# Kernel tuning notes

Hardware: AMD Instinct MI355X
Metric: run time of the kernel (lower is better)

## Reference

```python
import jax, jax.numpy as jnp
import numpy as np

B, T, F, N = 262144, 3, 17, 8
EMBD = 32
DT = 0.2  # 25/5*0.04
EPS = 1e-8  # torch.cosine_similarity eps


def _mono(x, wi, bi, wo, bo):
    # monotonic_fun with increasing=False: relu(-Linear(x)) -> Linear
    h = jax.nn.relu(-(x @ wi.T + bi))  # (..., EMBD)
    return h @ wo.T + bo               # (..., 1)


def _cos(a, b):
    dot = jnp.sum(a * b, axis=-1)
    na = jnp.maximum(jnp.linalg.norm(a, axis=-1), EPS)
    nb = jnp.maximum(jnp.linalg.norm(b, axis=-1), EPS)
    return dot / (na * nb)


def _angle_clamp(vec, e, ang):
    # vec: (B,K,2), e: (B,2) -> keep forces within effective angle cone, sum over K
    keep = jnp.abs(_cos(e[:, None, :], vec)) > ang
    return jnp.sum(vec * keep[..., None], axis=1)


def setup_inputs() -> dict:
    key = jax.random.key(0)
    ks = jax.random.split(key, 8)
    ego = jax.random.normal(ks[0], (B, T, F), jnp.float32)
    ego = ego.at[:, :, 2:4].multiply(10.0)  # position scale
    nei = jax.random.normal(ks[1], (B, N, F), jnp.float32)
    nei = nei.at[:, :, 2:4].multiply(10.0).at[:, :, 4:6].multiply(0.1)
    border = jax.random.normal(ks[2], (4,), jnp.float32)
    attr_dest_para = jax.random.uniform(ks[3], (2,), jnp.float32) + 0.1  # relu(rand), keep away from 0 divisor
    eff_angle = jax.nn.sigmoid(jax.random.uniform(ks[4], (1,), jnp.float32))

    def mlp(k):
        k1, k2, k3, k4 = jax.random.split(k, 4)
        wi = jax.random.uniform(k1, (EMBD, 1), jnp.float32)      # clamped >= 0
        bi = jax.random.normal(k2, (EMBD,), jnp.float32) * 0.1
        wo = jax.random.uniform(k3, (1, EMBD), jnp.float32) * 0.1  # clamped >= 0
        bo = jax.random.normal(k4, (1,), jnp.float32) * 0.1
        return wi, bi, wo, bo

    an = mlp(ks[5])
    rn = mlp(ks[6])
    rb = mlp(ks[7])
    dl = mlp(jax.random.fold_in(key, 99))
    return dict(
        ego=ego, nei=nei, border=border,
        attr_dest_para=attr_dest_para, eff_angle=eff_angle,
        an_wi=an[0], an_bi=an[1], an_wo=an[2], an_bo=an[3],
        rn_wi=rn[0], rn_bi=rn[1], rn_wo=rn[2], rn_bo=rn[3],
        rb_wi=rb[0], rb_bi=rb[1], rb_wo=rb[2], rb_bo=rb[3],
        dl_wi=dl[0], dl_bi=dl[1], dl_wo=dl[2], dl_bo=dl[3],
    )


def reference(ego, nei, border, attr_dest_para, eff_angle,
              an_wi, an_bi, an_wo, an_bo,
              rn_wi, rn_bi, rn_wo, rn_bo,
              rb_wi, rb_bi, rb_wo, rb_bo,
              dl_wi, dl_bi, dl_wo, dl_bo):
    ego_last = ego[:, -1]  # (B,F)

    # --- attr_destination (desired_velocity=None branch) ---
    v34 = ego_last[:, 3:5]
    dv = jnp.stack([jnp.linalg.norm(v34, axis=-1),
                    jnp.zeros(ego.shape[0], ego.dtype)], axis=1)  # (B,2)
    f_dest = ((attr_dest_para[1] * dv - v34) / attr_dest_para[0])[:, None, :]  # (B,1,2)

    # --- attr_repu_neighbors ---
    r = nei[:, :, 2:4] - ego_last[:, None, 2:4]  # (B,N,2)
    mask = nei[:, :, 2:4] == 0                    # (B,N,2)
    r_norm = jnp.linalg.norm(r, axis=-1, keepdims=True)  # (B,N,1)

    # neighbor durality: quirky use of batch element 1, shared across batch
    ids_last = ego[1, -1, 8:-1]  # (8,) neighbor-id columns
    dur = jnp.zeros(N, ego.dtype)
    for t in range(ego.shape[1]):
        dur = dur + jnp.isin(ids_last, ego[1, t, 8:-1]).astype(ego.dtype)

    f_attr = _mono(r_norm, an_wi, an_bi, an_wo, an_bo) * r / r_norm \
             * _mono(dur[:, None], dl_wi, dl_bi, dl_wo, dl_bo)  # (B,N,2)*(N,1)
    f_attr = jnp.where(mask, 0.0, f_attr)

    v_nei = nei[:, :, 4:6]
    b = r_norm \
        + jnp.sum((r + v_nei * DT) ** 2, axis=-1, keepdims=True) \
        - jnp.sum((v_nei * DT) ** 2, axis=-1, keepdims=True)
    b = jnp.sqrt(b) / 2
    f_repu = _mono(b, rn_wi, rn_bi, rn_wo, rn_bo) * r / r_norm
    f_repu = jnp.where(mask, 0.0, f_repu)

    # --- repu_borders (select_lane = [0, -1]) ---
    rb_all = ego_last[:, 3, None] - border        # (B,4)
    rbv = jnp.stack([rb_all[:, 0], rb_all[:, -1]], axis=1)  # (B,2)
    rbn = jnp.abs(rbv)
    f_bor = _mono(rbn[..., None], rb_wi, rb_bi, rb_wo, rb_bo) * (rbv / rbn)[..., None]  # (B,2,1)
    f_bor = jnp.concatenate([jnp.zeros_like(f_bor), f_bor], axis=-1)  # (B,2,2): [0, fy]

    # --- angle clamp + integrate ---
    e = ego_last[:, 4:6]
    e = e / jnp.linalg.norm(e, axis=1, keepdims=True)
    a = (_angle_clamp(f_dest, e, eff_angle)
         + _angle_clamp(f_attr, e, eff_angle) + _angle_clamp(f_repu, e, eff_angle)
         + _angle_clamp(f_bor, e, eff_angle))
    v = ego_last[:, 2:4] + a * DT
    s = ego_last[:, :2] + v * DT
    return jnp.concatenate([s, v, a], axis=1)  # (B,6)
```

## Files before the change

kernel.cpp:

```cpp
#include <hip/hip_runtime.h>

#define DTC 0.2f
#define EPSC 1e-8f


__device__ __forceinline__ float mono_eval(const float* __restrict__ kn, float x) {
    int i = (kn[15] <= x) ? 16 : 0;
    i += (kn[i + 7] <= x) ? 8 : 0;
    i += (kn[i + 3] <= x) ? 4 : 0;
    i += (kn[i + 1] <= x) ? 2 : 0;
    i += (kn[i] <= x) ? 1 : 0;
    return -fmaf(kn[32 + i], x, kn[65 + i]);
}

__global__ __launch_bounds__(256, 6) void sfm_fused(
    const float* __restrict__ ego, const float* __restrict__ nei,
    const float* __restrict__ border, const float* __restrict__ adp,
    const float* __restrict__ eang,
    const float* __restrict__ an_wi, const float* __restrict__ an_bi,
    const float* __restrict__ an_wo, const float* __restrict__ an_bo,
    const float* __restrict__ rn_wi, const float* __restrict__ rn_bi,
    const float* __restrict__ rn_wo, const float* __restrict__ rn_bo,
    const float* __restrict__ rb_wi, const float* __restrict__ rb_bi,
    const float* __restrict__ rb_wo, const float* __restrict__ rb_bo,
    const float* __restrict__ dl_wi, const float* __restrict__ dl_bi,
    const float* __restrict__ dl_wo, const float* __restrict__ dl_bo,
    float* __restrict__ out, int Bn)
{
    __shared__ __align__(16) float sw[360];
    __shared__ __align__(16) float snei[4352];
    __shared__ __align__(16) float sego[1632];
    __shared__ __align__(16) float sout[192];

    int t = threadIdx.x;

    if (t < 96) {
        int f = t >> 5, k = t & 31;
        const float* wip = (f == 0) ? an_wi : ((f == 1) ? rn_wi : rb_wi);
        const float* bip = (f == 0) ? an_bi : ((f == 1) ? rn_bi : rb_bi);
        const float* wop = (f == 0) ? an_wo : ((f == 1) ? rn_wo : rb_wo);
        float wi = wip[k], bi = bip[k], wo = wop[k];
        snei[t]       = -bi / wi;
        snei[96 + t]  = wi * wo;
        snei[192 + t] = wo * bi;
    }
    __syncthreads();
    if (t < 96) {
        int f = t >> 5, k = t & 31;
        float my = snei[t];
        int rank = 0;
        for (int m = 0; m < 32; ++m) {
            float o = snei[f * 32 + m];
            rank += (o < my || (o == my && m < k)) ? 1 : 0;
        }
        snei[288 + f * 32 + rank] = my;
        snei[384 + f * 32 + rank] = snei[96 + t];
        snei[480 + f * 32 + rank] = snei[192 + t];
    }
    __syncthreads();
    if (t < 96) {
        int f = t >> 5, p = t & 31;
        float sw_ = 0.f, sb_ = 0.f;
        for (int m = p; m < 32; ++m) { sw_ += snei[384 + f * 32 + m]; sb_ += snei[480 + f * 32 + m]; }
        int base = 16 + f * 112;
        sw[base + p]      = snei[288 + f * 32 + p];
        sw[base + 32 + p] = sw_;
        sw[base + 65 + p] = sb_;
        if (p == 0) { sw[base + 64] = 0.f; sw[base + 97] = 0.f; }
    }
    if (t >= 96 && t < 104) {
        int j = t - 96;
        const float* base = ego + 51;
        float idv = base[2 * 17 + 8 + j];
        float dur = 0.f;
        for (int tt = 0; tt < 3; ++tt) {
            bool fo = false;
            for (int m = 0; m < 8; ++m) fo = fo || (idv == base[tt * 17 + 8 + m]);
            dur += fo ? 1.f : 0.f;
        }
        float acc = 0.f;
        for (int k = 0; k < 32; ++k)
            acc = fmaf(dl_wo[k], fmaxf(0.f, -fmaf(dl_wi[k], dur, dl_bi[k])), acc);
        sw[j] = acc + dl_bo[0];
    }
    if (t == 104) sw[352] = an_bo[0];
    if (t == 105) sw[353] = rn_bo[0];
    if (t == 106) sw[354] = rb_bo[0];
    if (t == 107) sw[355] = adp[0];
    if (t == 108) sw[356] = adp[1];
    if (t == 109) sw[357] = eang[0];
    if (t == 110) sw[358] = border[0];
    if (t == 111) sw[359] = border[3];
    __syncthreads();

    int l   = t & 7;
    int r32 = t >> 3;
    long long nTiles = ((long long)Bn + 31) >> 5;

    for (long long tt = blockIdx.x; tt < nTiles; tt += gridDim.x) {
        {
            const float4* nsrc = (const float4*)nei + tt * 1088;
            float4* nd = (float4*)snei;
#pragma unroll
            for (int i = 0; i < 5; ++i) {
                int idx = t + 256 * i;
                if (idx < 1088 && tt * 1088 + idx < (long long)Bn * 34) nd[idx] = nsrc[idx];
            }
            const float4* esrc = (const float4*)ego + tt * 408;
            float4* ed = (float4*)sego;
#pragma unroll
            for (int i = 0; i < 2; ++i) {
                int idx = t + 256 * i;
                if (idx < 408 && tt * 408 + idx < ((long long)Bn * 51) / 4) ed[idx] = esrc[idx];
            }
        }
        __syncthreads();

        long long row = tt * 32 + r32;
        if (row < Bn) {
            const float* eg = sego + 51 * r32 + 34;
            float g0 = eg[0], g1 = eg[1], g2 = eg[2], g3 = eg[3], g4 = eg[4], g5 = eg[5];

            const float* nr = snei + 136 * r32 + 17 * l + 2;
            float nx = nr[0], ny = nr[1], vx = nr[2], vy = nr[3];

            float Rx = nx - g2, Ry = ny - g3;
            float rr = sqrtf(Rx * Rx + Ry * Ry);
            float ax = fmaf(vx, DTC, Rx), ay = fmaf(vy, DTC, Ry);
            float wx = vx * DTC, wy = vy * DTC;
            float bb = sqrtf(rr + ax * ax + ay * ay - wx * wx - wy * wy) * 0.5f;

            float an_bo_v = sw[352], rn_bo_v = sw[353], rb_bo_v = sw[354];
            float p0 = sw[355], p1 = sw[356], ang = sw[357];
            float rb0 = g3 - sw[358], rb1 = g3 - sw[359];
            float rbn0 = fabsf(rb0), rbn1 = fabsf(rb1);

            float fA = mono_eval(sw + 16, rr) + an_bo_v;
            float fR = mono_eval(sw + 128, bb) + rn_bo_v;
            float xb = (l == 1) ? rbn1 : rbn0;
            float vB = 0.f;
            if (l < 2) vB = mono_eval(sw + 240, xb) + rb_bo_v;
            int lb = (t & 63) & ~7;
            float vB0 = __shfl(vB, lb + 0, 64);
            float vB1 = __shfl(vB, lb + 1, 64);

            float elen = sqrtf(g4 * g4 + g5 * g5);
            float ex = g4 / elen, ey = g5 / elen;
            float na = fmaxf(sqrtf(ex * ex + ey * ey), EPSC);

            float axs = 0.f, ays = 0.f;
#define CLAMP_ADD(VX, VY)                                                   \
            {                                                               \
                float _vx = (VX), _vy = (VY);                               \
                float _nv = fmaxf(sqrtf(_vx * _vx + _vy * _vy), EPSC);      \
                float _c = (ex * _vx + ey * _vy) / (na * _nv);              \
                if (fabsf(_c) > ang) { axs += _vx; ays += _vy; }            \
            }

            float mfx = (nx == 0.f) ? 0.f : 1.f;
            float mfy = (ny == 0.f) ? 0.f : 1.f;

            { float coef = fA / rr * sw[l];  CLAMP_ADD(coef * Rx * mfx, coef * Ry * mfy); }
            { float coef = fR / rr;          CLAMP_ADD(coef * Rx * mfx, coef * Ry * mfy); }

#pragma unroll
            for (int m = 1; m < 8; m <<= 1) {
                axs += __shfl_xor(axs, m, 64);
                ays += __shfl_xor(ays, m, 64);
            }

            if (l == 0) {
                float dvn = sqrtf(g3 * g3 + g4 * g4);
                CLAMP_ADD((p1 * dvn - g3) / p0, -g4 / p0);
                CLAMP_ADD(0.f, vB0 * (rb0 / rbn0));
                CLAMP_ADD(0.f, vB1 * (rb1 / rbn1));

                float vxo = fmaf(axs, DTC, g2);
                float vyo = fmaf(ays, DTC, g3);
                float* op = sout + 6 * r32;
                op[0] = fmaf(vxo, DTC, g0);
                op[1] = fmaf(vyo, DTC, g1);
                op[2] = vxo; op[3] = vyo;
                op[4] = axs; op[5] = ays;
            }
#undef CLAMP_ADD
        }
        __syncthreads();

        if (t < 48) {
            long long o4 = tt * 48 + t;
            if (o4 < ((long long)Bn * 6) / 4) ((float4*)out)[o4] = ((const float4*)sout)[t];
        }
        __syncthreads();
    }
}

extern "C" void kernel_launch(void* const* d_in, const int* in_sizes, int n_in,
                              void* d_out, int out_size, void* d_ws, size_t ws_size,
                              hipStream_t stream) {
    const float* ego    = (const float*)d_in[0];
    const float* nei    = (const float*)d_in[1];
    const float* border = (const float*)d_in[2];
    const float* adp    = (const float*)d_in[3];
    const float* eang   = (const float*)d_in[4];
    const float* an_wi  = (const float*)d_in[5];
    const float* an_bi  = (const float*)d_in[6];
    const float* an_wo  = (const float*)d_in[7];
    const float* an_bo  = (const float*)d_in[8];
    const float* rn_wi  = (const float*)d_in[9];
    const float* rn_bi  = (const float*)d_in[10];
    const float* rn_wo  = (const float*)d_in[11];
    const float* rn_bo  = (const float*)d_in[12];
    const float* rb_wi  = (const float*)d_in[13];
    const float* rb_bi  = (const float*)d_in[14];
    const float* rb_wo  = (const float*)d_in[15];
    const float* rb_bo  = (const float*)d_in[16];
    const float* dl_wi  = (const float*)d_in[17];
    const float* dl_bi  = (const float*)d_in[18];
    const float* dl_wo  = (const float*)d_in[19];
    const float* dl_bo  = (const float*)d_in[20];
    float* out = (float*)d_out;
    (void)d_ws; (void)ws_size;

    int Bn = in_sizes[0] / (3 * 17);

    sfm_fused<<<1536, 256, 0, stream>>>(ego, nei, border, adp, eang,
                                        an_wi, an_bi, an_wo, an_bo,
                                        rn_wi, rn_bi, rn_wo, rn_bo,
                                        rb_wi, rb_bi, rb_wo, rb_bo,
                                        dl_wi, dl_bi, dl_wo, dl_bo,
                                        out, Bn);
}
```

Baseline: 284.1 us.

## Replace LDS-staged tile loop with direct register loads and one-shot grid

Drops the shared-memory staging of full nei/ego tiles and instead has each thread load only the fields it needs (positions/velocities of its neighbor, one ego field distributed via shuffles) for four rows up front. The persistent grid-stride loop with barriers is replaced by a grid sized to cover all rows, and outputs are written directly instead of through LDS. This cuts LDS usage and block-wide barriers and issues loads early for latency hiding, but reads are now strided, partially used cache lines instead of coalesced float4 tiles, and the per-block weight-table setup is repeated across many more blocks.

```diff
diff --git a/kernel.cpp b/kernel.cpp
--- a/kernel.cpp
+++ b/kernel.cpp
@@ -13,7 +13,7 @@
     return -fmaf(kn[32 + i], x, kn[65 + i]);
 }
 
-__global__ __launch_bounds__(256, 6) void sfm_fused(
+__global__ __launch_bounds__(256) void sfm_fused(
     const float* __restrict__ ego, const float* __restrict__ nei,
     const float* __restrict__ border, const float* __restrict__ adp,
     const float* __restrict__ eang,
@@ -28,9 +28,7 @@
     float* __restrict__ out, int Bn)
 {
     __shared__ __align__(16) float sw[360];
-    __shared__ __align__(16) float snei[4352];
-    __shared__ __align__(16) float sego[1632];
-    __shared__ __align__(16) float sout[192];
+    __shared__ __align__(16) float scr[576];
 
     int t = threadIdx.x;
 
@@ -40,30 +38,30 @@
         const float* bip = (f == 0) ? an_bi : ((f == 1) ? rn_bi : rb_bi);
         const float* wop = (f == 0) ? an_wo : ((f == 1) ? rn_wo : rb_wo);
         float wi = wip[k], bi = bip[k], wo = wop[k];
-        snei[t]       = -bi / wi;
-        snei[96 + t]  = wi * wo;
-        snei[192 + t] = wo * bi;
+        scr[t]       = -bi / wi;
+        scr[96 + t]  = wi * wo;
+        scr[192 + t] = wo * bi;
     }
     __syncthreads();
     if (t < 96) {
         int f = t >> 5, k = t & 31;
-        float my = snei[t];
+        float my = scr[t];
         int rank = 0;
         for (int m = 0; m < 32; ++m) {
-            float o = snei[f * 32 + m];
+            float o = scr[f * 32 + m];
             rank += (o < my || (o == my && m < k)) ? 1 : 0;
         }
-        snei[288 + f * 32 + rank] = my;
-        snei[384 + f * 32 + rank] = snei[96 + t];
-        snei[480 + f * 32 + rank] = snei[192 + t];
+        scr[288 + f * 32 + rank] = my;
+        scr[384 + f * 32 + rank] = scr[96 + t];
+        scr[480 + f * 32 + rank] = scr[192 + t];
     }
     __syncthreads();
     if (t < 96) {
         int f = t >> 5, p = t & 31;
         float sw_ = 0.f, sb_ = 0.f;
-        for (int m = p; m < 32; ++m) { sw_ += snei[384 + f * 32 + m]; sb_ += snei[480 + f * 32 + m]; }
+        for (int m = p; m < 32; ++m) { sw_ += scr[384 + f * 32 + m]; sb_ += scr[480 + f * 32 + m]; }
         int base = 16 + f * 112;
-        sw[base + p]      = snei[288 + f * 32 + p];
+        sw[base + p]      = scr[288 + f * 32 + p];
         sw[base + 32 + p] = sw_;
         sw[base + 65 + p] = sb_;
         if (p == 0) { sw[base + 64] = 0.f; sw[base + 97] = 0.f; }
@@ -93,105 +91,95 @@
     if (t == 111) sw[359] = border[3];
     __syncthreads();
 
-    int l   = t & 7;
-    int r32 = t >> 3;
-    long long nTiles = ((long long)Bn + 31) >> 5;
-
-    for (long long tt = blockIdx.x; tt < nTiles; tt += gridDim.x) {
-        {
-            const float4* nsrc = (const float4*)nei + tt * 1088;
-            float4* nd = (float4*)snei;
+    int l  = t & 7;
+    int g  = t >> 3;
+    long long base_row = (long long)blockIdx.x * 128 + g;
+
+    float egv[4], nx[4], ny[4], vx[4], vy[4];
 #pragma unroll
-            for (int i = 0; i < 5; ++i) {
-                int idx = t + 256 * i;
-                if (idx < 1088 && tt * 1088 + idx < (long long)Bn * 34) nd[idx] = nsrc[idx];
-            }
-            const float4* esrc = (const float4*)ego + tt * 408;
-            float4* ed = (float4*)sego;
+    for (int i = 0; i < 4; ++i) {
+        long long row = base_row + 32 * i;
+        long long rc = (row < Bn) ? row : (Bn - 1);
+        egv[i] = ego[rc * 51 + 34 + ((l < 6) ? l : 0)];
+        const float* nr = nei + rc * 136 + 17 * l + 2;
+        nx[i] = nr[0]; ny[i] = nr[1]; vx[i] = nr[2]; vy[i] = nr[3];
+    }
+
+    float an_bo_v = sw[352], rn_bo_v = sw[353], rb_bo_v = sw[354];
+    float p0 = sw[355], p1 = sw[356], ang = sw[357];
+    float bor0 = sw[358], bor3 = sw[359];
+    float dlf_l = sw[l];
+    int lb = (t & 63) & ~7;
+
 #pragma unroll
-            for (int i = 0; i < 2; ++i) {
-                int idx = t + 256 * i;
-                if (idx < 408 && tt * 408 + idx < ((long long)Bn * 51) / 4) ed[idx] = esrc[idx];
-            }
-        }
-        __syncthreads();
-
-        long long row = tt * 32 + r32;
-        if (row < Bn) {
-            const float* eg = sego + 51 * r32 + 34;
-            float g0 = eg[0], g1 = eg[1], g2 = eg[2], g3 = eg[3], g4 = eg[4], g5 = eg[5];
-
-            const float* nr = snei + 136 * r32 + 17 * l + 2;
-            float nx = nr[0], ny = nr[1], vx = nr[2], vy = nr[3];
-
-            float Rx = nx - g2, Ry = ny - g3;
-            float rr = sqrtf(Rx * Rx + Ry * Ry);
-            float ax = fmaf(vx, DTC, Rx), ay = fmaf(vy, DTC, Ry);
-            float wx = vx * DTC, wy = vy * DTC;
-            float bb = sqrtf(rr + ax * ax + ay * ay - wx * wx - wy * wy) * 0.5f;
-
-            float an_bo_v = sw[352], rn_bo_v = sw[353], rb_bo_v = sw[354];
-            float p0 = sw[355], p1 = sw[356], ang = sw[357];
-            float rb0 = g3 - sw[358], rb1 = g3 - sw[359];
-            float rbn0 = fabsf(rb0), rbn1 = fabsf(rb1);
-
-            float fA = mono_eval(sw + 16, rr) + an_bo_v;
-            float fR = mono_eval(sw + 128, bb) + rn_bo_v;
-            float xb = (l == 1) ? rbn1 : rbn0;
-            float vB = 0.f;
-            if (l < 2) vB = mono_eval(sw + 240, xb) + rb_bo_v;
-            int lb = (t & 63) & ~7;
-            float vB0 = __shfl(vB, lb + 0, 64);
-            float vB1 = __shfl(vB, lb + 1, 64);
-
-            float elen = sqrtf(g4 * g4 + g5 * g5);
-            float ex = g4 / elen, ey = g5 / elen;
-            float na = fmaxf(sqrtf(ex * ex + ey * ey), EPSC);
-
-            float axs = 0.f, ays = 0.f;
+    for (int i = 0; i < 4; ++i) {
+        long long row = base_row + 32 * i;
+        if (row >= Bn) break;
+
+        float g0 = __shfl(egv[i], lb + 0, 64);
+        float g1 = __shfl(egv[i], lb + 1, 64);
+        float g2 = __shfl(egv[i], lb + 2, 64);
+        float g3 = __shfl(egv[i], lb + 3, 64);
+        float g4 = __shfl(egv[i], lb + 4, 64);
+        float g5 = __shfl(egv[i], lb + 5, 64);
+
+        float Rx = nx[i] - g2, Ry = ny[i] - g3;
+        float rr = sqrtf(Rx * Rx + Ry * Ry);
+        float ax = fmaf(vx[i], DTC, Rx), ay = fmaf(vy[i], DTC, Ry);
+        float wx = vx[i] * DTC, wy = vy[i] * DTC;
+        float bb = sqrtf(rr + ax * ax + ay * ay - wx * wx - wy * wy) * 0.5f;
+
+        float rb0 = g3 - bor0, rb1 = g3 - bor3;
+        float rbn0 = fabsf(rb0), rbn1 = fabsf(rb1);
+
+        float fA = mono_eval(sw + 16, rr) + an_bo_v;
+        float fR = mono_eval(sw + 128, bb) + rn_bo_v;
+        float xb = (l == 1) ? rbn1 : rbn0;
+        float vB = 0.f;
+        if (l < 2) vB = mono_eval(sw + 240, xb) + rb_bo_v;
+        float vB0 = __shfl(vB, lb + 0, 64);
+        float vB1 = __shfl(vB, lb + 1, 64);
+
+        float elen = sqrtf(g4 * g4 + g5 * g5);
+        float ex = g4 / elen, ey = g5 / elen;
+        float na = fmaxf(sqrtf(ex * ex + ey * ey), EPSC);
+
+        float axs = 0.f, ays = 0.f;
 #define CLAMP_ADD(VX, VY)                                                   \
-            {                                                               \
-                float _vx = (VX), _vy = (VY);                               \
-                float _nv = fmaxf(sqrtf(_vx * _vx + _vy * _vy), EPSC);      \
-                float _c = (ex * _vx + ey * _vy) / (na * _nv);              \
-                if (fabsf(_c) > ang) { axs += _vx; ays += _vy; }            \
-            }
-
-            float mfx = (nx == 0.f) ? 0.f : 1.f;
-            float mfy = (ny == 0.f) ? 0.f : 1.f;
-
-            { float coef = fA / rr * sw[l];  CLAMP_ADD(coef * Rx * mfx, coef * Ry * mfy); }
-            { float coef = fR / rr;          CLAMP_ADD(coef * Rx * mfx, coef * Ry * mfy); }
+        {                                                                   \
+            float _vx = (VX), _vy = (VY);                                   \
+            float _nv = fmaxf(sqrtf(_vx * _vx + _vy * _vy), EPSC);          \
+            float _c = (ex * _vx + ey * _vy) / (na * _nv);                  \
+            if (fabsf(_c) > ang) { axs += _vx; ays += _vy; }                \
+        }
+
+        float mfx = (nx[i] == 0.f) ? 0.f : 1.f;
+        float mfy = (ny[i] == 0.f) ? 0.f : 1.f;
+
+        { float coef = fA / rr * dlf_l;  CLAMP_ADD(coef * Rx * mfx, coef * Ry * mfy); }
+        { float coef = fR / rr;          CLAMP_ADD(coef * Rx * mfx, coef * Ry * mfy); }
 
 #pragma unroll
-            for (int m = 1; m < 8; m <<= 1) {
-                axs += __shfl_xor(axs, m, 64);
-                ays += __shfl_xor(ays, m, 64);
-            }
-
-            if (l == 0) {
-                float dvn = sqrtf(g3 * g3 + g4 * g4);
-                CLAMP_ADD((p1 * dvn - g3) / p0, -g4 / p0);
-                CLAMP_ADD(0.f, vB0 * (rb0 / rbn0));
-                CLAMP_ADD(0.f, vB1 * (rb1 / rbn1));
-
-                float vxo = fmaf(axs, DTC, g2);
-                float vyo = fmaf(ays, DTC, g3);
-                float* op = sout + 6 * r32;
-                op[0] = fmaf(vxo, DTC, g0);
-                op[1] = fmaf(vyo, DTC, g1);
-                op[2] = vxo; op[3] = vyo;
-                op[4] = axs; op[5] = ays;
-            }
+        for (int m = 1; m < 8; m <<= 1) {
+            axs += __shfl_xor(axs, m, 64);
+            ays += __shfl_xor(ays, m, 64);
+        }
+
+        if (l == 0) {
+            float dvn = sqrtf(g3 * g3 + g4 * g4);
+            CLAMP_ADD((p1 * dvn - g3) / p0, -g4 / p0);
+            CLAMP_ADD(0.f, vB0 * (rb0 / rbn0));
+            CLAMP_ADD(0.f, vB1 * (rb1 / rbn1));
+
+            float vxo = fmaf(axs, DTC, g2);
+            float vyo = fmaf(ays, DTC, g3);
+            float* op = out + row * 6;
+            op[0] = fmaf(vxo, DTC, g0);
+            op[1] = fmaf(vyo, DTC, g1);
+            op[2] = vxo; op[3] = vyo;
+            op[4] = axs; op[5] = ays;
+        }
 #undef CLAMP_ADD
-        }
-        __syncthreads();
-
-        if (t < 48) {
-            long long o4 = tt * 48 + t;
-            if (o4 < ((long long)Bn * 6) / 4) ((float4*)out)[o4] = ((const float4*)sout)[t];
-        }
-        __syncthreads();
     }
 }
 
@@ -224,7 +212,8 @@
 
     int Bn = in_sizes[0] / (3 * 17);
 
-    sfm_fused<<<1536, 256, 0, stream>>>(ego, nei, border, adp, eang,
+    int grid = (Bn + 127) / 128;
+    sfm_fused<<<grid, 256, 0, stream>>>(ego, nei, border, adp, eang,
                                         an_wi, an_bi, an_wo, an_bo,
                                         rn_wi, rn_bi, rn_wo, rn_bo,
                                         rb_wi, rb_bi, rb_wo, rb_bo,
```

New measurement: 282.6 us. About the same (-0.5%).
